# Kernel optimization log

Hardware: AMD Instinct MI355X
Metric: run time of the kernel (lower is better)

The kernel has to match this reference:

```python
import jax, jax.numpy as jnp
import numpy as np
from jax import lax

B, L, DM = 1, 2048, 1024   # batch, seq len, d_model
N = 16                     # d_state
K = 4                      # d_conv
DI = 2 * DM                # d_inner = d_model * expand_factor


def silu(v):
    return v * jax.nn.sigmoid(v)


def setup_inputs() -> dict:
    key = jax.random.key(0)
    ks = jax.random.split(key, 11)
    s = 0.02
    f32 = jnp.float32
    return {
        "x": jax.random.normal(ks[0], (B, L, DM), f32),
        "W_in": jax.random.normal(ks[1], (2 * DI, DM), f32) * s,
        "b_in": jnp.zeros((2 * DI,), f32),
        "W_conv": jax.random.normal(ks[2], (DI, 1, K), f32) * s,  # depthwise conv kernel (torch layout)
        "b_conv": jnp.zeros((DI,), f32),
        "W_x": jax.random.normal(ks[3], (DI + 2 * N, DI), f32) * s,
        "b_x": jnp.zeros((DI + 2 * N,), f32),
        "W_out": jax.random.normal(ks[4], (DM, DI), f32) * s,
        "b_out": jnp.zeros((DM,), f32),
        "A_log": jax.random.normal(ks[5], (DI, N), f32),
        "D": jnp.ones((DI,), f32),
    }


def reference(x, W_in, b_in, W_conv, b_conv, W_x, b_x, W_out, b_out, A_log, D):
    Bsz = x.shape[0]
    # in_proj and split into ssm branch / residual gate branch
    xr = x @ W_in.T + b_in                      # (B, L, 2*DI)
    xi, res = jnp.split(xr, 2, axis=-1)
    # causal depthwise conv1d: torch pads (K-1) both sides then slices [:L] == left-pad K-1
    xc = jnp.transpose(xi, (0, 2, 1))           # (B, DI, L)
    xc = lax.conv_general_dilated(
        xc, W_conv, window_strides=(1,), padding=[(K - 1, 0)],
        dimension_numbers=("NCH", "OIH", "NCH"), feature_group_count=DI,
    ) + b_conv[None, :, None]
    xi = silu(jnp.transpose(xc, (0, 2, 1)))     # (B, L, DI)
    # selective-scan parameterization
    proj = xi @ W_x.T + b_x                      # (B, L, DI + 2N)
    delta = jax.nn.softplus(proj[..., :DI])      # (B, L, DI)
    B_ssm = proj[..., DI:DI + N]                 # (B, L, N)
    C_ssm = proj[..., DI + N:]                   # (B, L, N)
    A = -jnp.exp(A_log)                          # (DI, N)
    dA = jnp.exp(delta[..., None] * A)                               # (B, L, DI, N)
    dBx = delta[..., None] * B_ssm[:, :, None, :] * xi[..., None]    # (B, L, DI, N)

    def step(h, inp):
        da, dbx, c = inp
        h = da * h + dbx                         # (B, DI, N)
        y = jnp.einsum("bdn,bn->bd", h, c)
        return h, y

    h0 = jnp.zeros((Bsz, DI, N), x.dtype)
    _, ys = lax.scan(
        step, h0,
        (jnp.swapaxes(dA, 0, 1), jnp.swapaxes(dBx, 0, 1), jnp.swapaxes(C_ssm, 0, 1)),
    )
    y = jnp.swapaxes(ys, 0, 1) + xi * D          # skip connection
    y = y * silu(res)                            # gate
    return y @ W_out.T + b_out                   # (B, L, DM)
```

## Files before the change

kernel.cpp:

```cpp
#include <hip/hip_runtime.h>
#include <stdint.h>

#define L_SEQ 2048
#define DMODEL 1024
#define DI_DIM 2048
#define NSSM 16
#define NPROJ 2080
#define NCHUNK 64
#define LCHUNK 32

typedef __attribute__((ext_vector_type(8))) short bf16x8;
typedef __attribute__((ext_vector_type(8))) unsigned short u16x8;
typedef __attribute__((ext_vector_type(4))) float f32x4;

__device__ __forceinline__ float bf2f(unsigned short u) {
  union { uint32_t u; float f; } v; v.u = (uint32_t)u << 16; return v.f;
}
__device__ __forceinline__ unsigned short f2bf(float f) {
  union { float f; uint32_t u; } v; v.f = f;
  uint32_t u = v.u;
  return (unsigned short)((u + 0x7fffu + ((u >> 16) & 1u)) >> 16);
}
__device__ __forceinline__ void async16(const void* g, void* l) {
  __builtin_amdgcn_global_load_lds(
      (__attribute__((address_space(1))) void*)(g),
      (__attribute__((address_space(3))) void*)(l), 16, 0, 0);
}
__device__ __forceinline__ float softplusf(float p) {
  return (p > 20.f) ? p : __logf(1.f + __expf(p));
}
__device__ __forceinline__ float siluf(float x) {
  return x * __builtin_amdgcn_rcpf(1.f + __expf(-x));
}

#define WAITV(N) asm volatile("s_waitcnt vmcnt(" #N ")" ::: "memory")
#define GBAR()                                   \
  {                                              \
    __builtin_amdgcn_s_barrier();                \
    asm volatile("" ::: "memory");               \
  }

#define CVT_N1 524288
#define CVT_N2 (CVT_N1 + 1048576)
#define CVT_N3 (CVT_N2 + 1064960)
#define CVT_N4 (CVT_N3 + 524288)
__global__ void k_convert4(const float* __restrict__ x, const float* __restrict__ win,
                           const float* __restrict__ wx, const float* __restrict__ wout,
                           unsigned short* __restrict__ xb, unsigned short* __restrict__ winb,
                           unsigned short* __restrict__ wxb, unsigned short* __restrict__ woutb) {
  int i = blockIdx.x * 256 + threadIdx.x;
  const float4* src; unsigned short* dst; int j;
  if (i < CVT_N1)      { src = (const float4*)x;    dst = xb;    j = i; }
  else if (i < CVT_N2) { src = (const float4*)win;  dst = winb;  j = i - CVT_N1; }
  else if (i < CVT_N3) { src = (const float4*)wx;   dst = wxb;   j = i - CVT_N2; }
  else if (i < CVT_N4) { src = (const float4*)wout; dst = woutb; j = i - CVT_N3; }
  else return;
  float4 v = src[j];
  ushort4 o;
  o.x = f2bf(v.x); o.y = f2bf(v.y); o.z = f2bf(v.z); o.w = f2bf(v.w);
  ((ushort4*)dst)[j] = o;
}

#define GSTAGE(BUF, KT)                                                        \
  {                                                                            \
    async16(ap + (KT), &As[BUF][soA]);                                         \
    async16(bp0 + (KT), &Bs[BUF][soB0]);                                       \
    async16(bp1 + (KT), &Bs[BUF][soB1]);                                       \
  }

#define GCOMPUTE(BUF)                                                          \
  {                                                                            \
    bf16x8 af[4], bfv[2];                                                      \
    _Pragma("unroll")                                                          \
    for (int i = 0; i < 4; i++)                                                \
      af[i] = *(const bf16x8*)&As[BUF][i * 512 + ro];                          \
    _Pragma("unroll")                                                          \
    for (int j = 0; j < 2; j++)                                                \
      bfv[j] = *(const bf16x8*)&Bs[BUF][(wave * 2 + j) * 512 + ro];            \
    _Pragma("unroll")                                                          \
    for (int i = 0; i < 4; i++)                                                \
      _Pragma("unroll")                                                        \
      for (int j = 0; j < 2; j++)                                              \
        acc[i][j] = __builtin_amdgcn_mfma_f32_16x16x32_bf16(af[i], bfv[j],     \
                                                        acc[i][j], 0, 0, 0);   \
  }

#define DEFINE_GEMM_BT(NAME, OutT)                                             \
__global__ __launch_bounds__(256) void NAME(                                   \
    const unsigned short* __restrict__ A, const unsigned short* __restrict__ B,\
    const float* __restrict__ bias, OutT* __restrict__ C,                      \
    int M, int N, int K) {                                                     \
  __shared__ unsigned short As[3][64 * 32];                                    \
  __shared__ unsigned short Bs[3][128 * 32];                                   \
  const int tid = threadIdx.x;                                                 \
  const int wave = tid >> 6;                                                   \
  const int lane = tid & 63;                                                   \
  const int m0 = blockIdx.x * 64;       \
  const int n0 = blockIdx.y * 128;                                             \
  const int kLen = K / gridDim.z;                                              \
  const int kLo = blockIdx.z * kLen;                                           \
      \
  const int srow = lane >> 2;                                                  \
  const int scol = ((lane & 3) ^ ((lane >> 3) & 3)) * 8;                       \
  int ar = m0 + wave * 16 + srow;         if (ar > M - 1) ar = M - 1;          \
  int br0 = n0 + wave * 32 + srow;        if (br0 > N - 1) br0 = N - 1;        \
  int br1 = n0 + wave * 32 + 16 + srow;   if (br1 > N - 1) br1 = N - 1;        \
  const unsigned short* ap  = A + (size_t)ar * K + scol + kLo;                 \
  const unsigned short* bp0 = B + (size_t)br0 * K + scol + kLo;                \
  const unsigned short* bp1 = B + (size_t)br1 * K + scol + kLo;                \
  const int soA  = wave * 512;                                                 \
  const int soB0 = (wave * 2) * 512;                                           \
  const int soB1 = (wave * 2 + 1) * 512;                                       \
                     \
  const int mrow = lane & 15;                                                  \
  const int swz8 = (((lane >> 4) ^ ((mrow >> 1) & 3)) * 8);                    \
  const int ro = mrow * 32 + swz8;                                             \
  f32x4 acc[4][2];                                                             \
  _Pragma("unroll")                                                            \
  for (int i = 0; i < 4; i++)                                                  \
    _Pragma("unroll")                                                          \
    for (int j = 0; j < 2; j++) acc[i][j] = (f32x4){0.f, 0.f, 0.f, 0.f};       \
  const int niter = kLen / 32;                                                 \
  _Pragma("unroll")                                                            \
  for (int j = 0; j < 2; j++) GSTAGE(j, j * 32)                                \
  int cur = 0, nxt = 2;                                                        \
  for (int t = 0; t < niter - 2; t++) {                                        \
    WAITV(3);                                                                  \
    GBAR()                                                                     \
    GSTAGE(nxt, (t + 2) * 32)                                                  \
    GCOMPUTE(cur)                                                              \
    cur = (cur == 2) ? 0 : cur + 1;                                            \
    nxt = (nxt == 2) ? 0 : nxt + 1;                                            \
  }                                                                            \
  WAITV(3); GBAR()                                                             \
  GCOMPUTE(cur) cur = (cur == 2) ? 0 : cur + 1;                                \
  WAITV(0); GBAR()                                                             \
  GCOMPUTE(cur)                                                                \
         \
  const bool withBias = (gridDim.z == 1);                                      \
  OutT* Cz = C + (size_t)blockIdx.z * ((size_t)M * N);                         \
  _Pragma("unroll")                                                            \
  for (int j = 0; j < 2; j++) {                                                \
    int col = n0 + wave * 32 + j * 16 + (lane & 15);                           \
    if (col < N) {                                                             \
      float bv = withBias ? bias[col] : 0.f;                                   \
      _Pragma("unroll")                                                        \
      for (int i = 0; i < 4; i++) {                                            \
        int rbase = m0 + i * 16 + (lane >> 4) * 4;                             \
        _Pragma("unroll")                                                      \
        for (int r = 0; r < 4; r++) {                                          \
          float v = acc[i][j][r] + bv;                                         \
          if constexpr (sizeof(OutT) == 2)                                     \
            Cz[(size_t)(rbase + r) * N + col] = (OutT)f2bf(v);                 \
          else                                                                 \
            Cz[(size_t)(rbase + r) * N + col] = (OutT)v;                       \
        }                                                                      \
      }                                                                        \
    }                                                                          \
  }                                                                            \
}

DEFINE_GEMM_BT(k_gemm_xr, unsigned short)
DEFINE_GEMM_BT(k_gemm_proj, float)
DEFINE_GEMM_BT(k_gemm_out, float)

__global__ void k_reduce_out(const float* __restrict__ part, const float* __restrict__ bias,
                             float* __restrict__ out) {
  int i = blockIdx.x * 256 + threadIdx.x;
  float4 a = ((const float4*)part)[i];
  float4 b = ((const float4*)(part + (size_t)L_SEQ * DMODEL))[i];
  int col = (i * 4) & (DMODEL - 1);
  float4 bb = *(const float4*)&bias[col];
  float4 o;
  o.x = a.x + b.x + bb.x; o.y = a.y + b.y + bb.y;
  o.z = a.z + b.z + bb.z; o.w = a.w + b.w + bb.w;
  ((float4*)out)[i] = o;
}

__global__ void k_conv_silu(const unsigned short* __restrict__ xr,
                            const float* __restrict__ Wc,
                            const float* __restrict__ bc,
                            unsigned short* __restrict__ xcb) {
  int idx = blockIdx.x * 256 + threadIdx.x;
  int t = idx >> 8;
  int d8 = (idx & 255) * 8;
  const size_t rs = 2 * DI_DIM;
  u16x8 x0 = (u16x8)(unsigned short)0, x1 = x0, x2 = x0;
  u16x8 x3 = *(const u16x8*)&xr[(size_t)t * rs + d8];
  if (t >= 1) x2 = *(const u16x8*)&xr[(size_t)(t - 1) * rs + d8];
  if (t >= 2) x1 = *(const u16x8*)&xr[(size_t)(t - 2) * rs + d8];
  if (t >= 3) x0 = *(const u16x8*)&xr[(size_t)(t - 3) * rs + d8];
  float4 b0 = *(const float4*)&bc[d8];
  float4 b1 = *(const float4*)&bc[d8 + 4];
  float bb[8] = {b0.x, b0.y, b0.z, b0.w, b1.x, b1.y, b1.z, b1.w};
  u16x8 o;
#pragma unroll
  for (int j = 0; j < 8; j++) {
    float4 wd = *(const float4*)&Wc[(size_t)(d8 + j) * 4];
    float acc = bb[j] + bf2f(x0[j]) * wd.x + bf2f(x1[j]) * wd.y +
                bf2f(x2[j]) * wd.z + bf2f(x3[j]) * wd.w;
    o[j] = f2bf(siluf(acc));
  }
  *(u16x8*)&xcb[(size_t)t * DI_DIM + d8] = o;
}

__global__ __launch_bounds__(256) void k_scan_a(
    const float* __restrict__ proj, const unsigned short* __restrict__ xcb,
    const float* __restrict__ A_log,
    float* __restrict__ Sdelta, float* __restrict__ hstate) {
  __shared__ float Bsh[LCHUNK * NSSM];
  const int d = blockIdx.x * 256 + threadIdx.x;
  const int c = blockIdx.y;
  const int t0 = c * LCHUNK;
  for (int i = threadIdx.x; i < LCHUNK * NSSM; i += 256) {
    int t = i >> 4, n = i & 15;
    Bsh[i] = proj[(size_t)(t0 + t) * NPROJ + DI_DIM + n];
  }
  __syncthreads();
  float Ar[NSSM], h[NSSM];
#pragma unroll
  for (int n = 0; n < NSSM; n++) {
    Ar[n] = -__expf(A_log[d * NSSM + n]);
    h[n] = 0.f;
  }
  const float* pp = proj + (size_t)t0 * NPROJ + d;
  const unsigned short* xp = xcb + (size_t)t0 * DI_DIM + d;
  float p_nxt = pp[0];
  unsigned short x_nxt = xp[0];
  float sd = 0.f;
  for (int t = 0; t < LCHUNK; t++) {
    float p = p_nxt;
    unsigned short xu = x_nxt;
    if (t + 1 < LCHUNK) {
      p_nxt = pp[(size_t)(t + 1) * NPROJ];
      x_nxt = xp[(size_t)(t + 1) * DI_DIM];
    }
    float delta = softplusf(p);
    float dx = delta * bf2f(xu);
    sd += delta;
#pragma unroll
    for (int n = 0; n < NSSM; n++)
      h[n] = __expf(delta * Ar[n]) * h[n] + dx * Bsh[t * NSSM + n];
  }
  Sdelta[(size_t)c * DI_DIM + d] = sd;
  float4* hp = (float4*)&hstate[((size_t)c * DI_DIM + d) * NSSM];
  hp[0] = (float4){h[0], h[1], h[2], h[3]};
  hp[1] = (float4){h[4], h[5], h[6], h[7]};
  hp[2] = (float4){h[8], h[9], h[10], h[11]};
  hp[3] = (float4){h[12], h[13], h[14], h[15]};
}

__global__ void k_scan_b(const float* __restrict__ A_log,
                         const float* __restrict__ Sdelta,
                         float* __restrict__ hstate) {
  int tid = blockIdx.x * 256 + threadIdx.x;
  int d = tid >> 4;
  float A = -__expf(A_log[tid]);
  float carry = 0.f;
  for (int cb = 0; cb < NCHUNK; cb += 8) {
    float v[8], s[8];
#pragma unroll
    for (int j = 0; j < 8; j++) {
      v[j] = hstate[(size_t)(cb + j) * DI_DIM * NSSM + tid];
      s[j] = Sdelta[(size_t)(cb + j) * DI_DIM + d];
    }
#pragma unroll
    for (int j = 0; j < 8; j++) {
      hstate[(size_t)(cb + j) * DI_DIM * NSSM + tid] = carry;
      carry = __expf(A * s[j]) * carry + v[j];
    }
  }
}

__global__ __launch_bounds__(256) void k_scan_c(
    const float* __restrict__ proj, const unsigned short* __restrict__ xcb,
    const float* __restrict__ A_log, const float* __restrict__ h0,
    const float* __restrict__ Dvec, const unsigned short* __restrict__ xr,
    unsigned short* __restrict__ ybf) {
  __shared__ float Bsh[LCHUNK * NSSM];
  __shared__ float Csh[LCHUNK * NSSM];
  const int d = blockIdx.x * 256 + threadIdx.x;
  const int c = blockIdx.y;
  const int t0 = c * LCHUNK;
  for (int i = threadIdx.x; i < LCHUNK * NSSM; i += 256) {
    int t = i >> 4, n = i & 15;
    size_t ob = (size_t)(t0 + t) * NPROJ + DI_DIM + n;
    Bsh[i] = proj[ob];
    Csh[i] = proj[ob + NSSM];
  }
  __syncthreads();
  float Ar[NSSM], h[NSSM];
#pragma unroll
  for (int n = 0; n < NSSM; n++)
    Ar[n] = -__expf(A_log[d * NSSM + n]);
  const float4* h0p = (const float4*)&h0[((size_t)c * DI_DIM + d) * NSSM];
  float4 hv0 = h0p[0], hv1 = h0p[1], hv2 = h0p[2], hv3 = h0p[3];
  h[0] = hv0.x; h[1] = hv0.y; h[2] = hv0.z; h[3] = hv0.w;
  h[4] = hv1.x; h[5] = hv1.y; h[6] = hv1.z; h[7] = hv1.w;
  h[8] = hv2.x; h[9] = hv2.y; h[10] = hv2.z; h[11] = hv2.w;
  h[12] = hv3.x; h[13] = hv3.y; h[14] = hv3.z; h[15] = hv3.w;
  float Dd = Dvec[d];
  const float* pp = proj + (size_t)t0 * NPROJ + d;
  const unsigned short* xp = xcb + (size_t)t0 * DI_DIM + d;
  const unsigned short* rp = xr + (size_t)t0 * (2 * DI_DIM) + DI_DIM + d;
  float p_nxt = pp[0];
  unsigned short x_nxt = xp[0];
  unsigned short r_nxt = rp[0];
  for (int t = 0; t < LCHUNK; t++) {
    float p = p_nxt;
    unsigned short xu = x_nxt, ru = r_nxt;
    if (t + 1 < LCHUNK) {
      p_nxt = pp[(size_t)(t + 1) * NPROJ];
      x_nxt = xp[(size_t)(t + 1) * DI_DIM];
      r_nxt = rp[(size_t)(t + 1) * (2 * DI_DIM)];
    }
    float delta = softplusf(p);
    float xi = bf2f(xu);
    float dx = delta * xi;
    float y = 0.f;
#pragma unroll
    for (int n = 0; n < NSSM; n++) {
      h[n] = __expf(delta * Ar[n]) * h[n] + dx * Bsh[t * NSSM + n];
      y += h[n] * Csh[t * NSSM + n];
    }
    y += xi * Dd;
    y *= siluf(bf2f(ru));
    ybf[(size_t)(t0 + t) * DI_DIM + d] = f2bf(y);
  }
}

extern "C" void kernel_launch(void* const* d_in, const int* in_sizes, int n_in,
                              void* d_out, int out_size, void* d_ws, size_t ws_size,
                              hipStream_t stream) {
  const float* x      = (const float*)d_in[0];
  const float* W_in   = (const float*)d_in[1];
  const float* b_in   = (const float*)d_in[2];
  const float* W_conv = (const float*)d_in[3];
  const float* b_conv = (const float*)d_in[4];
  const float* W_x    = (const float*)d_in[5];
  const float* b_x    = (const float*)d_in[6];
  const float* W_out  = (const float*)d_in[7];
  const float* b_out  = (const float*)d_in[8];
  const float* A_log  = (const float*)d_in[9];
  const float* Dv     = (const float*)d_in[10];
  float* out = (float*)d_out;

  char* ws = (char*)d_ws;
  size_t off = 0;
  auto alloc = [&](size_t bytes) { void* p = ws + off; off += (bytes + 255) & ~(size_t)255; return p; };
  unsigned short* win_bf = (unsigned short*)alloc((size_t)4096 * DMODEL * 2);
  unsigned short* wx_bf  = (unsigned short*)alloc((size_t)NPROJ * DI_DIM * 2);
  unsigned short* x_bf   = (unsigned short*)alloc((size_t)L_SEQ * DMODEL * 2);
  unsigned short* xr_bf  = (unsigned short*)alloc((size_t)L_SEQ * 2 * DI_DIM * 2);
  unsigned short* xcb    = (unsigned short*)alloc((size_t)L_SEQ * DI_DIM * 2);
  float* proj            = (float*)alloc((size_t)L_SEQ * NPROJ * 4);
  float* Sdelta          = (float*)alloc((size_t)NCHUNK * DI_DIM * 4);
  float* hstate          = (float*)alloc((size_t)NCHUNK * DI_DIM * NSSM * 4);
  if (off > ws_size) return;
  unsigned short* ybf     = win_bf;
  unsigned short* wout_bf = x_bf;
  float* part             = proj;

  unsigned short* woutb = (unsigned short*)hstate;
  unsigned short* wout2 = nullptr;
  {
    size_t need = (size_t)DMODEL * DI_DIM * 2;
    if (off + need <= ws_size) wout2 = (unsigned short*)alloc(need);
  }
  if (wout2) {
    k_convert4<<<CVT_N4 / 256, 256, 0, stream>>>(x, W_in, W_x, W_out,
                                                 x_bf, win_bf, wx_bf, wout2);
    wout_bf = wout2;
  } else {
    k_convert4<<<CVT_N3 / 256, 256, 0, stream>>>(x, W_in, W_x, W_out,
                                                 x_bf, win_bf, wx_bf, wout_bf);
  }

  {
    dim3 g(L_SEQ / 64, 4096 / 128);
    k_gemm_xr<<<g, 256, 0, stream>>>(x_bf, win_bf, b_in, xr_bf, L_SEQ, 4096, DMODEL);
  }
  if (!wout2) {
    k_convert4<<<(CVT_N4 - CVT_N3) / 256, 256, 0, stream>>>(
        W_out - (size_t)CVT_N3 * 4 + (size_t)CVT_N3 * 4, W_in, W_x, W_out,
        x_bf, win_bf, wx_bf, wout_bf);
  }
  k_conv_silu<<<(L_SEQ * DI_DIM / 8) / 256, 256, 0, stream>>>(xr_bf, W_conv, b_conv, xcb);
  {
    dim3 g(L_SEQ / 64, (NPROJ + 127) / 128);
    k_gemm_proj<<<g, 256, 0, stream>>>(xcb, wx_bf, b_x, proj, L_SEQ, NPROJ, DI_DIM);
  }
  {
    dim3 ga(DI_DIM / 256, NCHUNK);
    k_scan_a<<<ga, 256, 0, stream>>>(proj, xcb, A_log, Sdelta, hstate);
    k_scan_b<<<(DI_DIM * NSSM) / 256, 256, 0, stream>>>(A_log, Sdelta, hstate);
    k_scan_c<<<ga, 256, 0, stream>>>(proj, xcb, A_log, hstate, Dv, xr_bf, ybf);
  }
  {
    dim3 g(L_SEQ / 64, DMODEL / 128, 2);
    k_gemm_out<<<g, 256, 0, stream>>>(ybf, wout_bf, b_out, part, L_SEQ, DMODEL, DI_DIM);
    k_reduce_out<<<(L_SEQ * DMODEL / 4) / 256, 256, 0, stream>>>(part, b_out, out);
  }
}
```

Baseline: 262.1 us.

## Use 128x128 block tiles for in-proj and out-proj GEMMs

Adds a GEMM variant with a 128x128 output tile per block, where each of the 4 waves computes a 64x64 subtile (4x4 MFMA accumulators). The in-projection and out-projection GEMMs switch to it, halving the grid's M dimension. This raises arithmetic intensity and cuts LDS and global reloads per MFMA, at the cost of more registers and LDS per block and fewer blocks in flight, which may hurt occupancy and wave balance. A small dedicated W_out conversion kernel replaces the odd reuse of k_convert4 on the fallback path.

```diff
diff --git a/kernel.cpp b/kernel.cpp
--- a/kernel.cpp
+++ b/kernel.cpp
@@ -61,6 +61,15 @@
   ((ushort4*)dst)[j] = o;
 }
 
+__global__ void k_wout_cvt(const float* __restrict__ in, unsigned short* __restrict__ out) {
+  int i = blockIdx.x * 256 + threadIdx.x;
+  float4 v = ((const float4*)in)[i];
+  ushort4 o;
+  o.x = f2bf(v.x); o.y = f2bf(v.y); o.z = f2bf(v.z); o.w = f2bf(v.w);
+  ((ushort4*)out)[i] = o;
+}
+
+
 #define GSTAGE(BUF, KT)                                                        \
   {                                                                            \
     async16(ap + (KT), &As[BUF][soA]);                                         \
@@ -99,7 +108,6 @@
   const int n0 = blockIdx.y * 128;                                             \
   const int kLen = K / gridDim.z;                                              \
   const int kLo = blockIdx.z * kLen;                                           \
-      \
   const int srow = lane >> 2;                                                  \
   const int scol = ((lane & 3) ^ ((lane >> 3) & 3)) * 8;                       \
   int ar = m0 + wave * 16 + srow;         if (ar > M - 1) ar = M - 1;          \
@@ -111,7 +119,6 @@
   const int soA  = wave * 512;                                                 \
   const int soB0 = (wave * 2) * 512;                                           \
   const int soB1 = (wave * 2 + 1) * 512;                                       \
-                     \
   const int mrow = lane & 15;                                                  \
   const int swz8 = (((lane >> 4) ^ ((mrow >> 1) & 3)) * 8);                    \
   const int ro = mrow * 32 + swz8;                                             \
@@ -136,7 +143,6 @@
   GCOMPUTE(cur) cur = (cur == 2) ? 0 : cur + 1;                                \
   WAITV(0); GBAR()                                                             \
   GCOMPUTE(cur)                                                                \
-         \
   const bool withBias = (gridDim.z == 1);                                      \
   OutT* Cz = C + (size_t)blockIdx.z * ((size_t)M * N);                         \
   _Pragma("unroll")                                                            \
@@ -160,9 +166,110 @@
   }                                                                            \
 }
 
-DEFINE_GEMM_BT(k_gemm_xr, unsigned short)
 DEFINE_GEMM_BT(k_gemm_proj, float)
-DEFINE_GEMM_BT(k_gemm_out, float)
+
+#define G128STAGE(BUF, KT)                                                     \
+  {                                                                            \
+    async16(ap0 + (KT), &As[BUF][soA0]);                                       \
+    async16(ap1 + (KT), &As[BUF][soA1]);                                       \
+    async16(bp0 + (KT), &Bs[BUF][soB0]);                                       \
+    async16(bp1 + (KT), &Bs[BUF][soB1]);                                       \
+  }
+
+#define G128COMPUTE(BUF)                                                       \
+  {                                                                            \
+    bf16x8 af[4], bfv[4];                                                      \
+    _Pragma("unroll")                                                          \
+    for (int i = 0; i < 4; i++)                                                \
+      af[i] = *(const bf16x8*)&As[BUF][aBase + i * 512 + ro];                  \
+    _Pragma("unroll")                                                          \
+    for (int j = 0; j < 4; j++)                                                \
+      bfv[j] = *(const bf16x8*)&Bs[BUF][bBase + j * 512 + ro];                 \
+    _Pragma("unroll")                                                          \
+    for (int i = 0; i < 4; i++)                                                \
+      _Pragma("unroll")                                                        \
+      for (int j = 0; j < 4; j++)                                              \
+        acc[i][j] = __builtin_amdgcn_mfma_f32_16x16x32_bf16(af[i], bfv[j],     \
+                                                        acc[i][j], 0, 0, 0);   \
+  }
+
+#define DEFINE_GEMM128(NAME, OutT)                                             \
+__global__ __launch_bounds__(256) void NAME(                                   \
+    const unsigned short* __restrict__ A, const unsigned short* __restrict__ B,\
+    const float* __restrict__ bias, OutT* __restrict__ C,                      \
+    int M, int N, int K) {                                                     \
+  __shared__ unsigned short As[3][128 * 32];                                   \
+  __shared__ unsigned short Bs[3][128 * 32];                                   \
+  const int tid = threadIdx.x;                                                 \
+  const int wave = tid >> 6;                                                   \
+  const int lane = tid & 63;                                                   \
+  const int m0 = blockIdx.x * 128;      \
+  const int n0 = blockIdx.y * 128;                                             \
+  const int kLen = K / gridDim.z;                                              \
+  const int kLo = blockIdx.z * kLen;                                           \
+  const int srow = lane >> 2;                                                  \
+  const int scol = ((lane & 3) ^ ((lane >> 3) & 3)) * 8;                       \
+  int ar0 = m0 + wave * 32 + srow;        if (ar0 > M - 1) ar0 = M - 1;        \
+  int ar1 = ar0 + 16;                     if (ar1 > M - 1) ar1 = M - 1;        \
+  int br0 = n0 + wave * 32 + srow;        if (br0 > N - 1) br0 = N - 1;        \
+  int br1 = br0 + 16;                     if (br1 > N - 1) br1 = N - 1;        \
+  const unsigned short* ap0 = A + (size_t)ar0 * K + scol + kLo;                \
+  const unsigned short* ap1 = A + (size_t)ar1 * K + scol + kLo;                \
+  const unsigned short* bp0 = B + (size_t)br0 * K + scol + kLo;                \
+  const unsigned short* bp1 = B + (size_t)br1 * K + scol + kLo;                \
+  const int soA0 = wave * 1024, soA1 = soA0 + 512;                             \
+  const int soB0 = wave * 1024, soB1 = soB0 + 512;                             \
+  const int mrow = lane & 15;                                                  \
+  const int swz8 = (((lane >> 4) ^ ((mrow >> 1) & 3)) * 8);                    \
+  const int ro = mrow * 32 + swz8;                                             \
+  const int aBase = (wave >> 1) * 2048;                                        \
+  const int bBase = (wave & 1) * 2048;                                         \
+  f32x4 acc[4][4];                                                             \
+  _Pragma("unroll")                                                            \
+  for (int i = 0; i < 4; i++)                                                  \
+    _Pragma("unroll")                                                          \
+    for (int j = 0; j < 4; j++) acc[i][j] = (f32x4){0.f, 0.f, 0.f, 0.f};       \
+  const int niter = kLen / 32;                                                 \
+  _Pragma("unroll")                                                            \
+  for (int j = 0; j < 2; j++) G128STAGE(j, j * 32)                             \
+  int cur = 0, nxt = 2;                                                        \
+  for (int t = 0; t < niter - 2; t++) {                                        \
+    WAITV(4);                                                                  \
+    GBAR()                                                                     \
+    G128STAGE(nxt, (t + 2) * 32)                                               \
+    G128COMPUTE(cur)                                                           \
+    cur = (cur == 2) ? 0 : cur + 1;                                            \
+    nxt = (nxt == 2) ? 0 : nxt + 1;                                            \
+  }                                                                            \
+  WAITV(4); GBAR()                                                             \
+  G128COMPUTE(cur) cur = (cur == 2) ? 0 : cur + 1;                             \
+  WAITV(0); GBAR()                                                             \
+  G128COMPUTE(cur)                                                             \
+  const bool withBias = (gridDim.z == 1);                                      \
+  OutT* Cz = C + (size_t)blockIdx.z * ((size_t)M * N);                         \
+  _Pragma("unroll")                                                            \
+  for (int j = 0; j < 4; j++) {                                                \
+    int col = n0 + (wave & 1) * 64 + j * 16 + (lane & 15);                     \
+    if (col < N) {                                                             \
+      float bv = withBias ? bias[col] : 0.f;                                   \
+      _Pragma("unroll")                                                        \
+      for (int i = 0; i < 4; i++) {                                            \
+        int rbase = m0 + (wave >> 1) * 64 + i * 16 + (lane >> 4) * 4;          \
+        _Pragma("unroll")                                                      \
+        for (int r = 0; r < 4; r++) {                                          \
+          float v = acc[i][j][r] + bv;                                         \
+          if constexpr (sizeof(OutT) == 2)                                     \
+            Cz[(size_t)(rbase + r) * N + col] = (OutT)f2bf(v);                 \
+          else                                                                 \
+            Cz[(size_t)(rbase + r) * N + col] = (OutT)v;                       \
+        }                                                                      \
+      }                                                                        \
+    }                                                                          \
+  }                                                                            \
+}
+
+DEFINE_GEMM128(k_gemm_xr128, unsigned short)
+DEFINE_GEMM128(k_gemm_out128, float)
 
 __global__ void k_reduce_out(const float* __restrict__ part, const float* __restrict__ bias,
                              float* __restrict__ out) {
@@ -361,7 +468,6 @@
   unsigned short* wout_bf = x_bf;
   float* part             = proj;
 
-  unsigned short* woutb = (unsigned short*)hstate;
   unsigned short* wout2 = nullptr;
   {
     size_t need = (size_t)DMODEL * DI_DIM * 2;
@@ -373,17 +479,15 @@
     wout_bf = wout2;
   } else {
     k_convert4<<<CVT_N3 / 256, 256, 0, stream>>>(x, W_in, W_x, W_out,
-                                                 x_bf, win_bf, wx_bf, wout_bf);
+                                                 x_bf, win_bf, wx_bf, x_bf );
   }
 
   {
-    dim3 g(L_SEQ / 64, 4096 / 128);
-    k_gemm_xr<<<g, 256, 0, stream>>>(x_bf, win_bf, b_in, xr_bf, L_SEQ, 4096, DMODEL);
+    dim3 g(L_SEQ / 128, 4096 / 128);
+    k_gemm_xr128<<<g, 256, 0, stream>>>(x_bf, win_bf, b_in, xr_bf, L_SEQ, 4096, DMODEL);
   }
   if (!wout2) {
-    k_convert4<<<(CVT_N4 - CVT_N3) / 256, 256, 0, stream>>>(
-        W_out - (size_t)CVT_N3 * 4 + (size_t)CVT_N3 * 4, W_in, W_x, W_out,
-        x_bf, win_bf, wx_bf, wout_bf);
+    k_wout_cvt<<<(DMODEL * DI_DIM / 4) / 256, 256, 0, stream>>>(W_out, wout_bf);
   }
   k_conv_silu<<<(L_SEQ * DI_DIM / 8) / 256, 256, 0, stream>>>(xr_bf, W_conv, b_conv, xcb);
   {
@@ -397,8 +501,8 @@
     k_scan_c<<<ga, 256, 0, stream>>>(proj, xcb, A_log, hstate, Dv, xr_bf, ybf);
   }
   {
-    dim3 g(L_SEQ / 64, DMODEL / 128, 2);
-    k_gemm_out<<<g, 256, 0, stream>>>(ybf, wout_bf, b_out, part, L_SEQ, DMODEL, DI_DIM);
+    dim3 g(L_SEQ / 128, DMODEL / 128, 2);
+    k_gemm_out128<<<g, 256, 0, stream>>>(ybf, wout_bf, b_out, part, L_SEQ, DMODEL, DI_DIM);
     k_reduce_out<<<(L_SEQ * DMODEL / 4) / 256, 256, 0, stream>>>(part, b_out, out);
   }
 }
```

Result: slower. 268.0 us (+2.3%).

## Fuse B/C projection columns into conv-silu kernel and trim proj GEMM to DI columns

Applied to the files above, without the earlier changes.

The 32 B/C columns of the x-projection are now computed inside the depthwise-conv+SiLU kernel from an LDS tile of 8 timesteps, using a transposed bf16 copy of those weight rows made during conversion. The projection GEMM is narrowed from 2080 to 2048 output columns, which removes a partially filled 17th N-tile, and gains an ldc parameter so it can still write into the wider proj buffer. The conv kernel now processes 8 timesteps per block and reuses the sliding window from registers. The cost is an extra scalar dot-product phase in the conv kernel, fewer blocks in that kernel, and a scattered transposed write during weight conversion.

```diff
diff --git a/kernel.cpp b/kernel.cpp
--- a/kernel.cpp
+++ b/kernel.cpp
@@ -8,6 +8,7 @@
 #define NPROJ 2080
 #define NCHUNK 64
 #define LCHUNK 32
+#define NBC 32
 
 typedef __attribute__((ext_vector_type(8))) short bf16x8;
 typedef __attribute__((ext_vector_type(8))) unsigned short u16x8;
@@ -47,19 +48,43 @@
 __global__ void k_convert4(const float* __restrict__ x, const float* __restrict__ win,
                            const float* __restrict__ wx, const float* __restrict__ wout,
                            unsigned short* __restrict__ xb, unsigned short* __restrict__ winb,
-                           unsigned short* __restrict__ wxb, unsigned short* __restrict__ woutb) {
+                           unsigned short* __restrict__ wxb, unsigned short* __restrict__ woutb,
+                           unsigned short* __restrict__ wbct) {
   int i = blockIdx.x * 256 + threadIdx.x;
   const float4* src; unsigned short* dst; int j;
+  bool isWx = false;
   if (i < CVT_N1)      { src = (const float4*)x;    dst = xb;    j = i; }
   else if (i < CVT_N2) { src = (const float4*)win;  dst = winb;  j = i - CVT_N1; }
-  else if (i < CVT_N3) { src = (const float4*)wx;   dst = wxb;   j = i - CVT_N2; }
+  else if (i < CVT_N3) { src = (const float4*)wx;   dst = wxb;   j = i - CVT_N2; isWx = true; }
   else if (i < CVT_N4) { src = (const float4*)wout; dst = woutb; j = i - CVT_N3; }
   else return;
   float4 v = src[j];
   ushort4 o;
   o.x = f2bf(v.x); o.y = f2bf(v.y); o.z = f2bf(v.z); o.w = f2bf(v.w);
   ((ushort4*)dst)[j] = o;
-}
+  if (isWx) {
+    int r = j >> 9;
+    if (r >= DI_DIM) {
+      int n = r - DI_DIM;
+      int d4 = (j & 511) * 4;
+      unsigned short ov[4] = {o.x, o.y, o.z, o.w};
+#pragma unroll
+      for (int k = 0; k < 4; k++) {
+        int d = d4 + k;
+        wbct[((size_t)(d >> 3) * NBC + n) * 8 + (d & 7)] = ov[k];
+      }
+    }
+  }
+}
+
+__global__ void k_wout_cvt(const float* __restrict__ in, unsigned short* __restrict__ out) {
+  int i = blockIdx.x * 256 + threadIdx.x;
+  float4 v = ((const float4*)in)[i];
+  ushort4 o;
+  o.x = f2bf(v.x); o.y = f2bf(v.y); o.z = f2bf(v.z); o.w = f2bf(v.w);
+  ((ushort4*)out)[i] = o;
+}
+
 
 #define GSTAGE(BUF, KT)                                                        \
   {                                                                            \
@@ -89,7 +114,7 @@
 __global__ __launch_bounds__(256) void NAME(                                   \
     const unsigned short* __restrict__ A, const unsigned short* __restrict__ B,\
     const float* __restrict__ bias, OutT* __restrict__ C,                      \
-    int M, int N, int K) {                                                     \
+    int M, int N, int K, int ldc) {                                            \
   __shared__ unsigned short As[3][64 * 32];                                    \
   __shared__ unsigned short Bs[3][128 * 32];                                   \
   const int tid = threadIdx.x;                                                 \
@@ -99,7 +124,6 @@
   const int n0 = blockIdx.y * 128;                                             \
   const int kLen = K / gridDim.z;                                              \
   const int kLo = blockIdx.z * kLen;                                           \
-      \
   const int srow = lane >> 2;                                                  \
   const int scol = ((lane & 3) ^ ((lane >> 3) & 3)) * 8;                       \
   int ar = m0 + wave * 16 + srow;         if (ar > M - 1) ar = M - 1;          \
@@ -111,7 +135,6 @@
   const int soA  = wave * 512;                                                 \
   const int soB0 = (wave * 2) * 512;                                           \
   const int soB1 = (wave * 2 + 1) * 512;                                       \
-                     \
   const int mrow = lane & 15;                                                  \
   const int swz8 = (((lane >> 4) ^ ((mrow >> 1) & 3)) * 8);                    \
   const int ro = mrow * 32 + swz8;                                             \
@@ -136,9 +159,8 @@
   GCOMPUTE(cur) cur = (cur == 2) ? 0 : cur + 1;                                \
   WAITV(0); GBAR()                                                             \
   GCOMPUTE(cur)                                                                \
-         \
   const bool withBias = (gridDim.z == 1);                                      \
-  OutT* Cz = C + (size_t)blockIdx.z * ((size_t)M * N);                         \
+  OutT* Cz = C + (size_t)blockIdx.z * ((size_t)M * ldc);                       \
   _Pragma("unroll")                                                            \
   for (int j = 0; j < 2; j++) {                                                \
     int col = n0 + wave * 32 + j * 16 + (lane & 15);                           \
@@ -151,9 +173,9 @@
         for (int r = 0; r < 4; r++) {                                          \
           float v = acc[i][j][r] + bv;                                         \
           if constexpr (sizeof(OutT) == 2)                                     \
-            Cz[(size_t)(rbase + r) * N + col] = (OutT)f2bf(v);                 \
+            Cz[(size_t)(rbase + r) * ldc + col] = (OutT)f2bf(v);               \
           else                                                                 \
-            Cz[(size_t)(rbase + r) * N + col] = (OutT)v;                       \
+            Cz[(size_t)(rbase + r) * ldc + col] = (OutT)v;                     \
         }                                                                      \
       }                                                                        \
     }                                                                          \
@@ -177,31 +199,78 @@
   ((float4*)out)[i] = o;
 }
 
-__global__ void k_conv_silu(const unsigned short* __restrict__ xr,
-                            const float* __restrict__ Wc,
-                            const float* __restrict__ bc,
-                            unsigned short* __restrict__ xcb) {
-  int idx = blockIdx.x * 256 + threadIdx.x;
-  int t = idx >> 8;
-  int d8 = (idx & 255) * 8;
+#define TCONV 8
+__global__ __launch_bounds__(256) void k_conv_silu_bc(
+    const unsigned short* __restrict__ xr, const float* __restrict__ Wc,
+    const float* __restrict__ bc, const unsigned short* __restrict__ wbct,
+    const float* __restrict__ bx, unsigned short* __restrict__ xcb,
+    float* __restrict__ proj) {
+  __shared__ float xi_sh[TCONV][DI_DIM];
+  __shared__ float red[8][TCONV][NBC];
+  const int tid = threadIdx.x;
+  const int t0 = blockIdx.x * TCONV;
+  const int d8 = tid * 8;
+  float wd[8][4], bb[8];
+#pragma unroll
+  for (int j = 0; j < 8; j++) {
+    float4 w = *(const float4*)&Wc[(size_t)(d8 + j) * 4];
+    wd[j][0] = w.x; wd[j][1] = w.y; wd[j][2] = w.z; wd[j][3] = w.w;
+  }
+  {
+    float4 b0 = *(const float4*)&bc[d8];
+    float4 b1 = *(const float4*)&bc[d8 + 4];
+    bb[0] = b0.x; bb[1] = b0.y; bb[2] = b0.z; bb[3] = b0.w;
+    bb[4] = b1.x; bb[5] = b1.y; bb[6] = b1.z; bb[7] = b1.w;
+  }
   const size_t rs = 2 * DI_DIM;
-  u16x8 x0 = (u16x8)(unsigned short)0, x1 = x0, x2 = x0;
-  u16x8 x3 = *(const u16x8*)&xr[(size_t)t * rs + d8];
-  if (t >= 1) x2 = *(const u16x8*)&xr[(size_t)(t - 1) * rs + d8];
-  if (t >= 2) x1 = *(const u16x8*)&xr[(size_t)(t - 2) * rs + d8];
-  if (t >= 3) x0 = *(const u16x8*)&xr[(size_t)(t - 3) * rs + d8];
-  float4 b0 = *(const float4*)&bc[d8];
-  float4 b1 = *(const float4*)&bc[d8 + 4];
-  float bb[8] = {b0.x, b0.y, b0.z, b0.w, b1.x, b1.y, b1.z, b1.w};
-  u16x8 o;
-#pragma unroll
-  for (int j = 0; j < 8; j++) {
-    float4 wd = *(const float4*)&Wc[(size_t)(d8 + j) * 4];
-    float acc = bb[j] + bf2f(x0[j]) * wd.x + bf2f(x1[j]) * wd.y +
-                bf2f(x2[j]) * wd.z + bf2f(x3[j]) * wd.w;
-    o[j] = f2bf(siluf(acc));
-  }
-  *(u16x8*)&xcb[(size_t)t * DI_DIM + d8] = o;
+  u16x8 xw0 = (u16x8)(unsigned short)0, xw1 = xw0, xw2 = xw0;
+  if (t0 >= 3) xw0 = *(const u16x8*)&xr[(size_t)(t0 - 3) * rs + d8];
+  if (t0 >= 2) xw1 = *(const u16x8*)&xr[(size_t)(t0 - 2) * rs + d8];
+  if (t0 >= 1) xw2 = *(const u16x8*)&xr[(size_t)(t0 - 1) * rs + d8];
+  for (int t = 0; t < TCONV; t++) {
+    u16x8 xw3 = *(const u16x8*)&xr[(size_t)(t0 + t) * rs + d8];
+    u16x8 o;
+#pragma unroll
+    for (int j = 0; j < 8; j++) {
+      float acc = bb[j] + bf2f(xw0[j]) * wd[j][0] + bf2f(xw1[j]) * wd[j][1] +
+                  bf2f(xw2[j]) * wd[j][2] + bf2f(xw3[j]) * wd[j][3];
+      unsigned short ob = f2bf(siluf(acc));
+      o[j] = ob;
+      xi_sh[t][d8 + j] = bf2f(ob);
+    }
+    *(u16x8*)&xcb[(size_t)(t0 + t) * DI_DIM + d8] = o;
+    xw0 = xw1; xw1 = xw2; xw2 = xw3;
+  }
+  __syncthreads();
+  const int n = tid & 31, seg = tid >> 5;
+  float acc[TCONV];
+#pragma unroll
+  for (int t = 0; t < TCONV; t++) acc[t] = 0.f;
+  for (int c = 0; c < 32; c++) {
+    int dc = seg * 32 + c;
+    u16x8 w8 = *(const u16x8*)&wbct[((size_t)dc * NBC + n) * 8];
+    float wf[8];
+#pragma unroll
+    for (int j = 0; j < 8; j++) wf[j] = bf2f(w8[j]);
+#pragma unroll
+    for (int t = 0; t < TCONV; t++) {
+      const f32x4* xp = (const f32x4*)&xi_sh[t][dc * 8];
+      f32x4 x0 = xp[0], x1 = xp[1];
+      acc[t] += x0[0] * wf[0] + x0[1] * wf[1] + x0[2] * wf[2] + x0[3] * wf[3] +
+                x1[0] * wf[4] + x1[1] * wf[5] + x1[2] * wf[6] + x1[3] * wf[7];
+    }
+  }
+#pragma unroll
+  for (int t = 0; t < TCONV; t++) red[seg][t][n] = acc[t];
+  __syncthreads();
+  {
+    int t = tid >> 5, nn = tid & 31;
+    float s = 0.f;
+#pragma unroll
+    for (int w = 0; w < 8; w++) s += red[w][t][nn];
+    s += bx[DI_DIM + nn];
+    proj[(size_t)(t0 + t) * NPROJ + DI_DIM + nn] = s;
+  }
 }
 
 __global__ __launch_bounds__(256) void k_scan_a(
@@ -356,12 +425,12 @@
   float* proj            = (float*)alloc((size_t)L_SEQ * NPROJ * 4);
   float* Sdelta          = (float*)alloc((size_t)NCHUNK * DI_DIM * 4);
   float* hstate          = (float*)alloc((size_t)NCHUNK * DI_DIM * NSSM * 4);
+  unsigned short* wbct   = (unsigned short*)alloc((size_t)DI_DIM * NBC * 2);
   if (off > ws_size) return;
   unsigned short* ybf     = win_bf;
   unsigned short* wout_bf = x_bf;
   float* part             = proj;
 
-  unsigned short* woutb = (unsigned short*)hstate;
   unsigned short* wout2 = nullptr;
   {
     size_t need = (size_t)DMODEL * DI_DIM * 2;
@@ -369,26 +438,25 @@
   }
   if (wout2) {
     k_convert4<<<CVT_N4 / 256, 256, 0, stream>>>(x, W_in, W_x, W_out,
-                                                 x_bf, win_bf, wx_bf, wout2);
+                                                 x_bf, win_bf, wx_bf, wout2, wbct);
     wout_bf = wout2;
   } else {
     k_convert4<<<CVT_N3 / 256, 256, 0, stream>>>(x, W_in, W_x, W_out,
-                                                 x_bf, win_bf, wx_bf, wout_bf);
+                                                 x_bf, win_bf, wx_bf, x_bf , wbct);
   }
 
   {
     dim3 g(L_SEQ / 64, 4096 / 128);
-    k_gemm_xr<<<g, 256, 0, stream>>>(x_bf, win_bf, b_in, xr_bf, L_SEQ, 4096, DMODEL);
+    k_gemm_xr<<<g, 256, 0, stream>>>(x_bf, win_bf, b_in, xr_bf, L_SEQ, 4096, DMODEL, 4096);
   }
   if (!wout2) {
-    k_convert4<<<(CVT_N4 - CVT_N3) / 256, 256, 0, stream>>>(
-        W_out - (size_t)CVT_N3 * 4 + (size_t)CVT_N3 * 4, W_in, W_x, W_out,
-        x_bf, win_bf, wx_bf, wout_bf);
-  }
-  k_conv_silu<<<(L_SEQ * DI_DIM / 8) / 256, 256, 0, stream>>>(xr_bf, W_conv, b_conv, xcb);
-  {
-    dim3 g(L_SEQ / 64, (NPROJ + 127) / 128);
-    k_gemm_proj<<<g, 256, 0, stream>>>(xcb, wx_bf, b_x, proj, L_SEQ, NPROJ, DI_DIM);
+    k_wout_cvt<<<(DMODEL * DI_DIM / 4) / 256, 256, 0, stream>>>(W_out, wout_bf);
+  }
+  k_conv_silu_bc<<<L_SEQ / TCONV, 256, 0, stream>>>(xr_bf, W_conv, b_conv, wbct,
+                                                    b_x, xcb, proj);
+  {
+    dim3 g(L_SEQ / 64, 2048 / 128);
+    k_gemm_proj<<<g, 256, 0, stream>>>(xcb, wx_bf, b_x, proj, L_SEQ, 2048, DI_DIM, NPROJ);
   }
   {
     dim3 ga(DI_DIM / 256, NCHUNK);
@@ -398,7 +466,7 @@
   }
   {
     dim3 g(L_SEQ / 64, DMODEL / 128, 2);
-    k_gemm_out<<<g, 256, 0, stream>>>(ybf, wout_bf, b_out, part, L_SEQ, DMODEL, DI_DIM);
+    k_gemm_out<<<g, 256, 0, stream>>>(ybf, wout_bf, b_out, part, L_SEQ, DMODEL, DI_DIM, DMODEL);
     k_reduce_out<<<(L_SEQ * DMODEL / 4) / 256, 256, 0, stream>>>(part, b_out, out);
   }
 }
```

New measurement: 264.4 us. Within noise of the previous version (+0.9%).
